# Kernel optimization log

Hardware: AMD Instinct MI355X
Metric: run time of the kernel (lower is better)

Reference implementation:

```python
import jax, jax.numpy as jnp
import numpy as np

B, T, D, UNITS = 32, 8192, 256, 128


def setup_inputs() -> dict:
    key = jax.random.key(0)
    ks = jax.random.split(key, 6)
    s = 0.05
    return {
        "query": jax.random.normal(ks[0], (B, D), dtype=jnp.float32),
        "values": jax.random.normal(ks[1], (B, T, D), dtype=jnp.float32),
        "W1_kernel": jax.random.normal(ks[2], (D, UNITS), dtype=jnp.float32) * s,
        "W1_bias": jnp.zeros((UNITS,), dtype=jnp.float32),
        "W2_kernel": jax.random.normal(ks[3], (D, UNITS), dtype=jnp.float32) * s,
        "W2_bias": jnp.zeros((UNITS,), dtype=jnp.float32),
        "V_kernel": jax.random.normal(ks[4], (UNITS, 1), dtype=jnp.float32) * s,
        "V_bias": jnp.zeros((1,), dtype=jnp.float32),
    }


def reference(query, values, W1_kernel, W1_bias, W2_kernel, W2_bias, V_kernel, V_bias):
    # W1(values): Dense with relu over last dim -> [B, T, U]
    h_v = jax.nn.relu(jnp.einsum('btd,du->btu', values, W1_kernel) + W1_bias)
    # W2(query) with time axis expanded -> [B, 1, U]
    h_q = jax.nn.relu(query @ W2_kernel + W2_bias)[:, None, :]
    # V(tanh(...)) -> score [B, T, 1]
    score = jnp.tanh(h_v + h_q) @ V_kernel + V_bias
    # softmax over the time axis
    attention_weights = jax.nn.softmax(score, axis=1)  # [B, T, 1]
    # weighted sum of values over T -> [B, D]
    context_vector = jnp.sum(attention_weights * values, axis=1)
    return context_vector, attention_weights
```

## Files before the change

kernel.cpp:

```cpp
#include <hip/hip_runtime.h>
#include <cmath>


#define B_ 32
#define T_ 8192
#define D_ 256
#define U_ 128
#define CH_ 64
#define NCH_ (T_ / CH_)
#define GRP_ 520

typedef float f32x4 __attribute__((ext_vector_type(4)));
typedef short s16x8 __attribute__((ext_vector_type(8)));
typedef __bf16 bf16x8 __attribute__((ext_vector_type(8)));

__device__ __forceinline__ float tanh_fast(float x) {
    float e = __expf(2.f * x);
    return 1.f - 2.f * __builtin_amdgcn_rcpf(e + 1.f);
}

__global__ __launch_bounds__(256) void prep(
    const float* __restrict__ W1, const float* __restrict__ query,
    const float* __restrict__ W2, const float* __restrict__ b2,
    unsigned short* __restrict__ W1h, unsigned short* __restrict__ W1l,
    float* __restrict__ hq)
{
    int blk = blockIdx.x, tid = threadIdx.x;
    if (blk < 128) {
        int idx2 = blk * 256 + tid;
        int k = idx2 >> 7, n = idx2 & 127;
        float wv = W1[idx2];
        int kk = k >> 5, j = k & 7, lg = (k >> 3) & 3;
        int lane = lg * 16 + (n & 15);
        int nn = n >> 4;
        int pos = ((kk * 8 + nn) * 64 + lane) * 8 + j;
        __bf16 hb = (__bf16)wv;
        float hf = (float)hb;
        __bf16 lb = (__bf16)(wv - hf);
        W1h[pos] = __builtin_bit_cast(unsigned short, hb);
        W1l[pos] = __builtin_bit_cast(unsigned short, lb);
    } else {
        __shared__ float hq2[256];
        int b = blk - 128;
        int u = tid & 127, half = tid >> 7;
        float acc = half ? 0.f : b2[u];
        const float* q = query + b * D_ + half * 128;
        const float* w2 = W2 + (half * 128) * U_ + u;
        for (int d = 0; d < 128; ++d)
            acc = fmaf(q[d], w2[d * U_], acc);
        hq2[tid] = acc;
        __syncthreads();
        if (tid < 128) hq[b * U_ + tid] = fmaxf(hq2[tid] + hq2[tid + 128], 0.f);
    }
}

__device__ __forceinline__ void stage_half(
    const float* __restrict__ src, int w, int lane,
    unsigned short* __restrict__ Ah, unsigned short* __restrict__ Al)
{
#pragma unroll
    for (int p = 0; p < 4; ++p) {
        int tile = w * 4 + p;
        int mt = tile >> 3, kk = tile & 7;
        const float* ptr = src + (mt * 16 + (lane & 15)) * D_ + kk * 32 + (lane >> 4) * 8;
        float4 x0 = *(const float4*)ptr;
        float4 x1 = *(const float4*)(ptr + 4);
        float xs[8] = {x0.x, x0.y, x0.z, x0.w, x1.x, x1.y, x1.z, x1.w};
        s16x8 hv, lv;
#pragma unroll
        for (int e = 0; e < 8; ++e) {
            __bf16 hb = (__bf16)xs[e];
            float hf = (float)hb;
            __bf16 lb = (__bf16)(xs[e] - hf);
            hv[e] = __builtin_bit_cast(short, hb);
            lv[e] = __builtin_bit_cast(short, lb);
        }
        int off = (mt * 8 + kk) * GRP_ + lane * 8;
        *(s16x8*)&Ah[off] = hv;
        *(s16x8*)&Al[off] = lv;
    }
}

__global__ __launch_bounds__(256, 2) void score_ctx(
    const float* __restrict__ values,
    const unsigned short* __restrict__ W1h, const unsigned short* __restrict__ W1l,
    const float* __restrict__ hq, const float* __restrict__ b1,
    const float* __restrict__ Vk,
    float* __restrict__ sc_g, float* __restrict__ st_g, float* __restrict__ cp_g)
{
    __shared__ __align__(16) unsigned short Ah[16 * GRP_];
    __shared__ __align__(16) unsigned short Al[16 * GRP_];
    __shared__ float scp[4][32];
    __shared__ float esc[32];
    __shared__ float m_s, l_s, alpha_s;

    const int tid = threadIdx.x;
    const int b = blockIdx.x >> 7;
    const int c = blockIdx.x & 127;
    const int t0 = c * CH_;
    const int lane = tid & 63;
    const int w = tid >> 6;
    const int u0 = lane & 15;

    if (tid == 0) { m_s = -1e30f; l_s = 0.f; }

    float b1v[2], hqv[2], Vv[2];
#pragma unroll
    for (int q = 0; q < 2; ++q) {
        int u = (2 * w + q) * 16 + u0;
        b1v[q] = b1[u];
        hqv[q] = hq[b * U_ + u];
        Vv[q] = Vk[u];
    }

    float c1 = 0.f;
    const float* vbase = values + ((size_t)b * T_ + t0) * D_;

    stage_half(vbase, w, lane, Ah, Al);

    for (int h = 0; h < 2; ++h) {
        __syncthreads();

        f32x4 acc[2][2];
#pragma unroll
        for (int mt = 0; mt < 2; ++mt)
#pragma unroll
            for (int q = 0; q < 2; ++q) acc[mt][q] = (f32x4){0.f, 0.f, 0.f, 0.f};

#pragma unroll
        for (int kk = 0; kk < 8; ++kk) {
            bf16x8 bh[2], bl[2];
#pragma unroll
            for (int q = 0; q < 2; ++q) {
                int nn = 2 * w + q;
                int boff = ((kk * 8 + nn) * 64 + lane) * 8;
                bh[q] = __builtin_bit_cast(bf16x8, *(const s16x8*)&W1h[boff]);
                bl[q] = __builtin_bit_cast(bf16x8, *(const s16x8*)&W1l[boff]);
            }
#pragma unroll
            for (int mt = 0; mt < 2; ++mt) {
                int aoff = (mt * 8 + kk) * GRP_ + lane * 8;
                bf16x8 ah = __builtin_bit_cast(bf16x8, *(const s16x8*)&Ah[aoff]);
                bf16x8 al = __builtin_bit_cast(bf16x8, *(const s16x8*)&Al[aoff]);
#pragma unroll
                for (int q = 0; q < 2; ++q) {
                    acc[mt][q] = __builtin_amdgcn_mfma_f32_16x16x32_bf16(ah, bh[q], acc[mt][q], 0, 0, 0);
                    acc[mt][q] = __builtin_amdgcn_mfma_f32_16x16x32_bf16(ah, bl[q], acc[mt][q], 0, 0, 0);
                    acc[mt][q] = __builtin_amdgcn_mfma_f32_16x16x32_bf16(al, bh[q], acc[mt][q], 0, 0, 0);
                }
            }
        }

#pragma unroll
        for (int mt = 0; mt < 2; ++mt) {
            float p[4];
#pragma unroll
            for (int i = 0; i < 4; ++i) {
                float z = 0.f;
#pragma unroll
                for (int q = 0; q < 2; ++q) {
                    float hpre = fmaxf(acc[mt][q][i] + b1v[q], 0.f) + hqv[q];
                    z += tanh_fast(hpre) * Vv[q];
                }
                p[i] = z;
            }
#pragma unroll
            for (int off = 1; off < 16; off <<= 1)
#pragma unroll
                for (int i = 0; i < 4; ++i) p[i] += __shfl_xor(p[i], off, 16);
            if (u0 == 0) {
                int base = mt * 16 + (lane >> 4) * 4;
#pragma unroll
                for (int i = 0; i < 4; ++i) scp[w][base + i] = p[i];
            }
        }
        __syncthreads();

        if (tid < 32) {
            float s = scp[0][tid] + scp[1][tid] + scp[2][tid] + scp[3][tid];
            sc_g[b * T_ + t0 + h * 32 + tid] = s;
            float mh = s;
#pragma unroll
            for (int off = 16; off >= 1; off >>= 1)
                mh = fmaxf(mh, __shfl_xor(mh, off, 32));
            float m_old = m_s;
            float m_new = fmaxf(m_old, mh);
            float e = __expf(s - m_new);
            esc[tid] = e;
            float lh = e;
#pragma unroll
            for (int off = 16; off >= 1; off >>= 1)
                lh += __shfl_xor(lh, off, 32);
            if (tid == 0) {
                alpha_s = __expf(m_old - m_new);
                l_s = l_s * alpha_s + lh;
                m_s = m_new;
            }
        }
        __syncthreads();

        {
            c1 *= alpha_s;
            const float* vcol = vbase + (size_t)(h * 32) * D_ + tid;
#pragma unroll
            for (int tl = 0; tl < 32; ++tl)
                c1 = fmaf(esc[tl], vcol[(size_t)tl * D_], c1);
        }
        if (h == 0) stage_half(vbase + 32 * D_, w, lane, Ah, Al);
    }

    cp_g[((size_t)(b * NCH_ + c)) * D_ + tid] = c1;
    if (tid == 0) {
        st_g[(b * NCH_ + c) * 2 + 0] = m_s;
        st_g[(b * NCH_ + c) * 2 + 1] = l_s;
    }
}

__global__ __launch_bounds__(256) void epilogue(
    const float* __restrict__ sc_g, const float* __restrict__ st_g,
    const float* __restrict__ cp_g, float* __restrict__ out)
{
    __shared__ float wcA[128];
    __shared__ float wm[4], wl[4];
    int blk = blockIdx.x, tid = threadIdx.x;
    int b = (blk < 256) ? (blk >> 3) : (blk - 256);

    float m_c = -1e30f, l_c = 0.f;
    if (tid < 128) {
        m_c = st_g[(b * NCH_ + tid) * 2 + 0];
        l_c = st_g[(b * NCH_ + tid) * 2 + 1];
    }
    float mm = m_c;
#pragma unroll
    for (int off = 32; off >= 1; off >>= 1) mm = fmaxf(mm, __shfl_xor(mm, off, 64));
    if ((tid & 63) == 0) wm[tid >> 6] = mm;
    __syncthreads();
    float M = fmaxf(fmaxf(wm[0], wm[1]), fmaxf(wm[2], wm[3]));
    float wc = (tid < 128) ? __expf(m_c - M) : 0.f;
    if (tid < 128) wcA[tid] = wc;
    float lw = l_c * wc;
#pragma unroll
    for (int off = 32; off >= 1; off >>= 1) lw += __shfl_xor(lw, off, 64);
    if ((tid & 63) == 0) wl[tid >> 6] = lw;
    __syncthreads();
    float invL = 1.f / (wl[0] + wl[1] + wl[2] + wl[3]);

    if (blk < 256) {
        int s8 = blk & 7;
        int t = s8 * 1024 + tid * 4;
        float4 s4 = *(const float4*)&sc_g[(size_t)b * T_ + t];
        float4 r;
        r.x = __expf(s4.x - M) * invL;
        r.y = __expf(s4.y - M) * invL;
        r.z = __expf(s4.z - M) * invL;
        r.w = __expf(s4.w - M) * invL;
        *(float4*)&out[B_ * D_ + (size_t)b * T_ + t] = r;
    } else {
        float a = 0.f;
        const float* p = cp_g + (size_t)b * NCH_ * D_ + tid;
#pragma unroll 8
        for (int c2 = 0; c2 < NCH_; ++c2)
            a = fmaf(wcA[c2], p[(size_t)c2 * D_], a);
        out[b * D_ + tid] = a * invL;
    }
}

extern "C" void kernel_launch(void* const* d_in, const int* in_sizes, int n_in,
                              void* d_out, int out_size, void* d_ws, size_t ws_size,
                              hipStream_t stream)
{
    const float* query = (const float*)d_in[0];
    const float* values = (const float*)d_in[1];
    const float* W1 = (const float*)d_in[2];
    const float* b1 = (const float*)d_in[3];
    const float* W2 = (const float*)d_in[4];
    const float* b2 = (const float*)d_in[5];
    const float* Vk = (const float*)d_in[6];
    float* out = (float*)d_out;
    char* ws = (char*)d_ws;

    float* scores = (float*)(ws + 0);
    float* hq     = (float*)(ws + 1048576);
    float* stats  = (float*)(ws + 1064960);
    float* ctxp   = (float*)(ws + 1097728);
    unsigned short* W1h = (unsigned short*)(ws + 5292032);
    unsigned short* W1l = (unsigned short*)(ws + 5357568);

    prep<<<160, 256, 0, stream>>>(W1, query, W2, b2, W1h, W1l, hq);
    score_ctx<<<B_ * NCH_, 256, 0, stream>>>(values, W1h, W1l, hq, b1, Vk,
                                             scores, stats, ctxp);
    epilogue<<<288, 256, 0, stream>>>(scores, stats, ctxp, out);
}
```

Measured before the change: 414.5 us.

## Restructure score kernel into 512-thread persistent chunks with double-buffered staging

Each block now has 8 waves and covers 256 timesteps instead of 64, with 1024 blocks instead of 4096. Each wave keeps its W1 hi/lo fragments in registers for the whole block rather than reloading them per half-chunk. LDS staging of the values tile is double-buffered so the next 32-row slice is loaded while the current one runs through MFMA. The online-softmax running max is removed and raw exp(score) is used, on the assumption that scores are bounded (|score| ≤ sum|V|). This simplifies the epilogue and the partial stats, but risks overflow if scores were ever large.

Result: faster. 391.8 us (-5.5%).

```diff
diff --git a/kernel.cpp b/kernel.cpp
--- a/kernel.cpp
+++ b/kernel.cpp
@@ -6,8 +6,7 @@
 #define T_ 8192
 #define D_ 256
 #define U_ 128
-#define CH_ 64
-#define NCH_ (T_ / CH_)
+#define NBC_ 32
 #define GRP_ 520
 
 typedef float f32x4 __attribute__((ext_vector_type(4)));
@@ -54,18 +53,29 @@
     }
 }
 
-__device__ __forceinline__ void stage_half(
-    const float* __restrict__ src, int w, int lane,
-    unsigned short* __restrict__ Ah, unsigned short* __restrict__ Al)
-{
-#pragma unroll
-    for (int p = 0; p < 4; ++p) {
-        int tile = w * 4 + p;
+__device__ __forceinline__ void stage_load(
+    const float* __restrict__ src, int w, int lane, float4 xr[2][2])
+{
+#pragma unroll
+    for (int p = 0; p < 2; ++p) {
+        int tile = w * 2 + p;
         int mt = tile >> 3, kk = tile & 7;
         const float* ptr = src + (mt * 16 + (lane & 15)) * D_ + kk * 32 + (lane >> 4) * 8;
-        float4 x0 = *(const float4*)ptr;
-        float4 x1 = *(const float4*)(ptr + 4);
-        float xs[8] = {x0.x, x0.y, x0.z, x0.w, x1.x, x1.y, x1.z, x1.w};
+        xr[p][0] = *(const float4*)ptr;
+        xr[p][1] = *(const float4*)(ptr + 4);
+    }
+}
+
+__device__ __forceinline__ void stage_store(
+    int w, int lane, const float4 xr[2][2],
+    unsigned short* __restrict__ Ah, unsigned short* __restrict__ Al)
+{
+#pragma unroll
+    for (int p = 0; p < 2; ++p) {
+        int tile = w * 2 + p;
+        int mt = tile >> 3, kk = tile & 7;
+        float xs[8] = {xr[p][0].x, xr[p][0].y, xr[p][0].z, xr[p][0].w,
+                       xr[p][1].x, xr[p][1].y, xr[p][1].z, xr[p][1].w};
         s16x8 hv, lv;
 #pragma unroll
         for (int e = 0; e < 8; ++e) {
@@ -81,73 +91,70 @@
     }
 }
 
-__global__ __launch_bounds__(256, 2) void score_ctx(
+__global__ __launch_bounds__(512, 2) void score_ctx(
     const float* __restrict__ values,
     const unsigned short* __restrict__ W1h, const unsigned short* __restrict__ W1l,
     const float* __restrict__ hq, const float* __restrict__ b1,
     const float* __restrict__ Vk,
     float* __restrict__ sc_g, float* __restrict__ st_g, float* __restrict__ cp_g)
 {
-    __shared__ __align__(16) unsigned short Ah[16 * GRP_];
-    __shared__ __align__(16) unsigned short Al[16 * GRP_];
-    __shared__ float scp[4][32];
+    __shared__ __align__(16) unsigned short AhB[2][16 * GRP_];
+    __shared__ __align__(16) unsigned short AlB[2][16 * GRP_];
+    __shared__ float scp[8][32];
     __shared__ float esc[32];
-    __shared__ float m_s, l_s, alpha_s;
+    __shared__ float cbuf[256];
 
     const int tid = threadIdx.x;
-    const int b = blockIdx.x >> 7;
-    const int c = blockIdx.x & 127;
-    const int t0 = c * CH_;
+    const int b = blockIdx.x >> 5;
+    const int blkc = blockIdx.x & 31;
     const int lane = tid & 63;
     const int w = tid >> 6;
     const int u0 = lane & 15;
 
-    if (tid == 0) { m_s = -1e30f; l_s = 0.f; }
-
-    float b1v[2], hqv[2], Vv[2];
-#pragma unroll
-    for (int q = 0; q < 2; ++q) {
-        int u = (2 * w + q) * 16 + u0;
-        b1v[q] = b1[u];
-        hqv[q] = hq[b * U_ + u];
-        Vv[q] = Vk[u];
-    }
-
+    bf16x8 bfh[8], bfl[8];
+#pragma unroll
+    for (int kk = 0; kk < 8; ++kk) {
+        int boff = ((kk * 8 + w) * 64 + lane) * 8;
+        bfh[kk] = __builtin_bit_cast(bf16x8, *(const s16x8*)&W1h[boff]);
+        bfl[kk] = __builtin_bit_cast(bf16x8, *(const s16x8*)&W1l[boff]);
+    }
+
+    const int u = w * 16 + u0;
+    const float b1v = b1[u];
+    const float hqv = hq[b * U_ + u];
+    const float Vv = Vk[u];
+
+    float l_acc = 0.f;
     float c1 = 0.f;
-    const float* vbase = values + ((size_t)b * T_ + t0) * D_;
-
-    stage_half(vbase, w, lane, Ah, Al);
-
-    for (int h = 0; h < 2; ++h) {
-        __syncthreads();
-
-        f32x4 acc[2][2];
-#pragma unroll
-        for (int mt = 0; mt < 2; ++mt)
-#pragma unroll
-            for (int q = 0; q < 2; ++q) acc[mt][q] = (f32x4){0.f, 0.f, 0.f, 0.f};
-
+    const int tb = blkc * 256;
+    const float* vblk = values + ((size_t)b * T_ + tb) * D_;
+
+    float4 xr[2][2];
+    stage_load(vblk, w, lane, xr);
+    stage_store(w, lane, xr, AhB[0], AlB[0]);
+    int cur = 0;
+
+#pragma unroll 2
+    for (int hh = 0; hh < 8; ++hh) {
+        __syncthreads();
+
+        if (hh < 7) stage_load(vblk + (size_t)(hh + 1) * 32 * D_, w, lane, xr);
+
+        const unsigned short* Ah = AhB[cur];
+        const unsigned short* Al = AlB[cur];
+        f32x4 acc[2];
+        acc[0] = (f32x4){0.f, 0.f, 0.f, 0.f};
+        acc[1] = (f32x4){0.f, 0.f, 0.f, 0.f};
 #pragma unroll
         for (int kk = 0; kk < 8; ++kk) {
-            bf16x8 bh[2], bl[2];
-#pragma unroll
-            for (int q = 0; q < 2; ++q) {
-                int nn = 2 * w + q;
-                int boff = ((kk * 8 + nn) * 64 + lane) * 8;
-                bh[q] = __builtin_bit_cast(bf16x8, *(const s16x8*)&W1h[boff]);
-                bl[q] = __builtin_bit_cast(bf16x8, *(const s16x8*)&W1l[boff]);
-            }
 #pragma unroll
             for (int mt = 0; mt < 2; ++mt) {
                 int aoff = (mt * 8 + kk) * GRP_ + lane * 8;
                 bf16x8 ah = __builtin_bit_cast(bf16x8, *(const s16x8*)&Ah[aoff]);
                 bf16x8 al = __builtin_bit_cast(bf16x8, *(const s16x8*)&Al[aoff]);
-#pragma unroll
-                for (int q = 0; q < 2; ++q) {
-                    acc[mt][q] = __builtin_amdgcn_mfma_f32_16x16x32_bf16(ah, bh[q], acc[mt][q], 0, 0, 0);
-                    acc[mt][q] = __builtin_amdgcn_mfma_f32_16x16x32_bf16(ah, bl[q], acc[mt][q], 0, 0, 0);
-                    acc[mt][q] = __builtin_amdgcn_mfma_f32_16x16x32_bf16(al, bh[q], acc[mt][q], 0, 0, 0);
-                }
+                acc[mt] = __builtin_amdgcn_mfma_f32_16x16x32_bf16(ah, bfh[kk], acc[mt], 0, 0, 0);
+                acc[mt] = __builtin_amdgcn_mfma_f32_16x16x32_bf16(ah, bfl[kk], acc[mt], 0, 0, 0);
+                acc[mt] = __builtin_amdgcn_mfma_f32_16x16x32_bf16(al, bfh[kk], acc[mt], 0, 0, 0);
             }
         }
 
@@ -156,13 +163,8 @@
             float p[4];
 #pragma unroll
             for (int i = 0; i < 4; ++i) {
-                float z = 0.f;
-#pragma unroll
-                for (int q = 0; q < 2; ++q) {
-                    float hpre = fmaxf(acc[mt][q][i] + b1v[q], 0.f) + hqv[q];
-                    z += tanh_fast(hpre) * Vv[q];
-                }
-                p[i] = z;
+                float hpre = fmaxf(acc[mt][i] + b1v, 0.f) + hqv;
+                p[i] = tanh_fast(hpre) * Vv;
             }
 #pragma unroll
             for (int off = 1; off < 16; off <<= 1)
@@ -177,90 +179,73 @@
         __syncthreads();
 
         if (tid < 32) {
-            float s = scp[0][tid] + scp[1][tid] + scp[2][tid] + scp[3][tid];
-            sc_g[b * T_ + t0 + h * 32 + tid] = s;
-            float mh = s;
-#pragma unroll
-            for (int off = 16; off >= 1; off >>= 1)
-                mh = fmaxf(mh, __shfl_xor(mh, off, 32));
-            float m_old = m_s;
-            float m_new = fmaxf(m_old, mh);
-            float e = __expf(s - m_new);
+            float s = 0.f;
+#pragma unroll
+            for (int ww = 0; ww < 8; ++ww) s += scp[ww][tid];
+            sc_g[(size_t)b * T_ + tb + hh * 32 + tid] = s;
+            float e = __expf(s);
             esc[tid] = e;
             float lh = e;
 #pragma unroll
             for (int off = 16; off >= 1; off >>= 1)
                 lh += __shfl_xor(lh, off, 32);
-            if (tid == 0) {
-                alpha_s = __expf(m_old - m_new);
-                l_s = l_s * alpha_s + lh;
-                m_s = m_new;
-            }
+            if (tid == 0) l_acc += lh;
         }
         __syncthreads();
 
         {
-            c1 *= alpha_s;
-            const float* vcol = vbase + (size_t)(h * 32) * D_ + tid;
-#pragma unroll
-            for (int tl = 0; tl < 32; ++tl)
-                c1 = fmaf(esc[tl], vcol[(size_t)tl * D_], c1);
-        }
-        if (h == 0) stage_half(vbase + 32 * D_, w, lane, Ah, Al);
-    }
-
-    cp_g[((size_t)(b * NCH_ + c)) * D_ + tid] = c1;
-    if (tid == 0) {
-        st_g[(b * NCH_ + c) * 2 + 0] = m_s;
-        st_g[(b * NCH_ + c) * 2 + 1] = l_s;
-    }
+            int colr = tid & 255, rh = tid >> 8;
+            const float* vcol = vblk + (size_t)(hh * 32 + rh * 16) * D_ + colr;
+#pragma unroll
+            for (int tl = 0; tl < 16; ++tl)
+                c1 = fmaf(esc[rh * 16 + tl], vcol[(size_t)tl * D_], c1);
+        }
+
+        if (hh < 7) stage_store(w, lane, xr, AhB[cur ^ 1], AlB[cur ^ 1]);
+        cur ^= 1;
+    }
+
+    if (tid >= 256) cbuf[tid - 256] = c1;
+    __syncthreads();
+    if (tid < 256)
+        cp_g[((size_t)(b * NBC_ + blkc)) * D_ + tid] = c1 + cbuf[tid];
+    if (tid == 0) st_g[b * NBC_ + blkc] = l_acc;
 }
 
 __global__ __launch_bounds__(256) void epilogue(
     const float* __restrict__ sc_g, const float* __restrict__ st_g,
     const float* __restrict__ cp_g, float* __restrict__ out)
 {
-    __shared__ float wcA[128];
-    __shared__ float wm[4], wl[4];
+    __shared__ float invL_s;
     int blk = blockIdx.x, tid = threadIdx.x;
     int b = (blk < 256) ? (blk >> 3) : (blk - 256);
 
-    float m_c = -1e30f, l_c = 0.f;
-    if (tid < 128) {
-        m_c = st_g[(b * NCH_ + tid) * 2 + 0];
-        l_c = st_g[(b * NCH_ + tid) * 2 + 1];
-    }
-    float mm = m_c;
-#pragma unroll
-    for (int off = 32; off >= 1; off >>= 1) mm = fmaxf(mm, __shfl_xor(mm, off, 64));
-    if ((tid & 63) == 0) wm[tid >> 6] = mm;
+    if (tid < 32) {
+        float l = st_g[b * NBC_ + tid];
+#pragma unroll
+        for (int off = 16; off >= 1; off >>= 1)
+            l += __shfl_xor(l, off, 32);
+        if (tid == 0) invL_s = 1.f / l;
+    }
     __syncthreads();
-    float M = fmaxf(fmaxf(wm[0], wm[1]), fmaxf(wm[2], wm[3]));
-    float wc = (tid < 128) ? __expf(m_c - M) : 0.f;
-    if (tid < 128) wcA[tid] = wc;
-    float lw = l_c * wc;
-#pragma unroll
-    for (int off = 32; off >= 1; off >>= 1) lw += __shfl_xor(lw, off, 64);
-    if ((tid & 63) == 0) wl[tid >> 6] = lw;
-    __syncthreads();
-    float invL = 1.f / (wl[0] + wl[1] + wl[2] + wl[3]);
+    float invL = invL_s;
 
     if (blk < 256) {
         int s8 = blk & 7;
         int t = s8 * 1024 + tid * 4;
         float4 s4 = *(const float4*)&sc_g[(size_t)b * T_ + t];
         float4 r;
-        r.x = __expf(s4.x - M) * invL;
-        r.y = __expf(s4.y - M) * invL;
-        r.z = __expf(s4.z - M) * invL;
-        r.w = __expf(s4.w - M) * invL;
+        r.x = __expf(s4.x) * invL;
+        r.y = __expf(s4.y) * invL;
+        r.z = __expf(s4.z) * invL;
+        r.w = __expf(s4.w) * invL;
         *(float4*)&out[B_ * D_ + (size_t)b * T_ + t] = r;
     } else {
         float a = 0.f;
-        const float* p = cp_g + (size_t)b * NCH_ * D_ + tid;
+        const float* p = cp_g + (size_t)b * NBC_ * D_ + tid;
 #pragma unroll 8
-        for (int c2 = 0; c2 < NCH_; ++c2)
-            a = fmaf(wcA[c2], p[(size_t)c2 * D_], a);
+        for (int c2 = 0; c2 < NBC_; ++c2)
+            a += p[(size_t)c2 * D_];
         out[b * D_ + tid] = a * invL;
     }
 }
@@ -282,12 +267,12 @@
     float* scores = (float*)(ws + 0);
     float* hq     = (float*)(ws + 1048576);
     float* stats  = (float*)(ws + 1064960);
-    float* ctxp   = (float*)(ws + 1097728);
-    unsigned short* W1h = (unsigned short*)(ws + 5292032);
-    unsigned short* W1l = (unsigned short*)(ws + 5357568);
+    float* ctxp   = (float*)(ws + 1069056);
+    unsigned short* W1h = (unsigned short*)(ws + 2117632);
+    unsigned short* W1l = (unsigned short*)(ws + 2183168);
 
     prep<<<160, 256, 0, stream>>>(W1, query, W2, b2, W1h, W1l, hq);
-    score_ctx<<<B_ * NCH_, 256, 0, stream>>>(values, W1h, W1l, hq, b1, Vk,
+    score_ctx<<<B_ * NBC_, 512, 0, stream>>>(values, W1h, W1l, hq, b1, Vk,
                                              scores, stats, ctxp);
     epilogue<<<288, 256, 0, stream>>>(scores, stats, ctxp, out);
 }
```
